# Kernel optimization log

Hardware: AMD Instinct MI355X
Metric: run time of the kernel (lower is better)

Reference implementation:

```python
import jax, jax.numpy as jnp
import numpy as np

ALPHA = 0.2  # LeakyReLU negative slope
NEG_INF = -9e15


def setup_inputs() -> dict:
    key = jax.random.key(0)
    k1, k2, k3, k4 = jax.random.split(key, 4)
    B, N, F_in, F_out = 8, 2048, 256, 128
    h = jax.random.normal(k1, (B, N, F_in), dtype=jnp.float32)
    adj = jax.random.randint(k2, (B, N, N), 0, 2, dtype=jnp.int32)
    # xavier_uniform with gain=1.414
    def xavier(k, shape, gain=1.414):
        fan_in, fan_out = shape[0], shape[1]
        limit = gain * np.sqrt(6.0 / (fan_in + fan_out))
        return jax.random.uniform(k, shape, jnp.float32, -limit, limit)
    W = xavier(k3, (F_in, F_out))
    a = xavier(k4, (2 * F_out, 1))
    return {"h": h, "adj": adj, "W": W, "a": a}


def reference(h, adj, W, a):
    # h: [B,N,F_in], adj: [B,N,N], W: [F_in,F_out], a: [2*F_out,1]
    Wh = jnp.einsum('bnf,fe->bne', h, W)  # [B,N,E]
    E = Wh.shape[-1]
    a_src, a_dst = a[:E, 0], a[E:, 0]
    # e[b,i,j] = leakyrelu(Wh[b,i].a_src + Wh[b,j].a_dst)  (additive decomposition
    # of a @ concat(Wh_i, Wh_j) -- same math, no [B,N,N,2E] intermediate)
    s_src = Wh @ a_src  # [B,N]
    s_dst = Wh @ a_dst  # [B,N]
    e = jax.nn.leaky_relu(s_src[:, :, None] + s_dst[:, None, :], negative_slope=ALPHA)
    e = jnp.where(adj > 0, e, NEG_INF)
    attention = jax.nn.softmax(e, axis=2)  # [B,N,N]
    # dropout p=0.0 / eval mode -> identity
    h_prime = jnp.einsum('bij,bje->bie', attention, Wh)
    return jax.nn.elu(h_prime)  # concat=True
```

## Files before the change

### kernel.cpp

```cpp
#include <hip/hip_runtime.h>
#include <hip/hip_bf16.h>

#define GAT_ALPHA 0.2f
#define LOG2E 1.4426950408889634f

typedef float f32x4 __attribute__((ext_vector_type(4)));
typedef int   i32x4 __attribute__((ext_vector_type(4)));
typedef short bf16x8 __attribute__((ext_vector_type(8)));

static constexpr int Nn  = 2048;
static constexpr int FIN = 256;
static constexpr int FO  = 128;

static __device__ __forceinline__ unsigned short f2bf(float x) {
    __hip_bfloat16 h = __float2bfloat16(x);
    return __builtin_bit_cast(unsigned short, h);
}
static __device__ __forceinline__ float bf2f(unsigned short u) {
    unsigned int v = ((unsigned int)u) << 16;
    return __builtin_bit_cast(float, v);
}

__global__ __launch_bounds__(256) void gat_prep(
        const float* __restrict__ W, const float* __restrict__ a,
        float* __restrict__ wa, unsigned int* __restrict__ md_key)
{
    __shared__ float pr[32][8];
    __shared__ float pd[32][8];
    const int t = threadIdx.x;
    const int kl = t >> 3, seg = t & 7;
    const int k = blockIdx.x * 32 + kl;
    float ps = 0.f, pv = 0.f;
    const float* wr = W + (size_t)k * FO + seg * 16;
    #pragma unroll
    for (int f = 0; f < 16; f += 4) {
        f32x4 wv = *(const f32x4*)(wr + f);
        f32x4 as = *(const f32x4*)(a + seg * 16 + f);
        f32x4 ad = *(const f32x4*)(a + FO + seg * 16 + f);
        ps += wv[0]*as[0] + wv[1]*as[1] + wv[2]*as[2] + wv[3]*as[3];
        pv += wv[0]*ad[0] + wv[1]*ad[1] + wv[2]*ad[2] + wv[3]*ad[3];
    }
    pr[kl][seg] = ps; pd[kl][seg] = pv;
    __syncthreads();
    if (t < 32) {
        float s = 0.f, d = 0.f;
        #pragma unroll
        for (int j = 0; j < 8; ++j) { s += pr[t][j]; d += pd[t][j]; }
        wa[blockIdx.x * 32 + t]       = s;
        wa[256 + blockIdx.x * 32 + t] = d;
    }
    if (blockIdx.x == 0 && t < 8) md_key[t] = 0u;
}

__global__ __launch_bounds__(256) void gat_wh(
        const float* __restrict__ h, const float* __restrict__ W,
        const float* __restrict__ wa, unsigned short* __restrict__ WhT,
        float* __restrict__ s_src, float* __restrict__ s_dst,
        unsigned int* __restrict__ md_key)
{
    __shared__ unsigned short WT[FO][264];
    __shared__ float wal[512];
    __shared__ float sred[64][4][2];
    __shared__ float red64[64];
    const int t  = threadIdx.x;
    const int b  = blockIdx.x & 7;
    const int n0 = (blockIdx.x >> 3) << 6;

    if (t < 128) *(f32x4*)&wal[t * 4] = *(const f32x4*)&wa[t * 4];
    #pragma unroll
    for (int c = 0; c < 32; ++c) {
        int flat = c * 1024 + t * 4;
        int k = flat >> 7, f = flat & 127;
        f32x4 wv = *(const f32x4*)&W[flat];
        WT[f + 0][k] = f2bf(wv[0]);
        WT[f + 1][k] = f2bf(wv[1]);
        WT[f + 2][k] = f2bf(wv[2]);
        WT[f + 3][k] = f2bf(wv[3]);
    }
    __syncthreads();

    {
        const int row = t >> 2, seg = t & 3;
        const float* hp  = h + ((size_t)(b * Nn + n0 + row)) * FIN + seg * 64;
        const float* was = &wal[seg * 64];
        const float* wad = &wal[256 + seg * 64];
        float ps = 0.f, pv = 0.f;
        #pragma unroll
        for (int j = 0; j < 64; j += 4) {
            f32x4 hv = *(const f32x4*)(hp + j);
            f32x4 sv = *(const f32x4*)(was + j);
            f32x4 dv = *(const f32x4*)(wad + j);
            ps += hv[0]*sv[0] + hv[1]*sv[1] + hv[2]*sv[2] + hv[3]*sv[3];
            pv += hv[0]*dv[0] + hv[1]*dv[1] + hv[2]*dv[2] + hv[3]*dv[3];
        }
        sred[row][seg][0] = ps;
        sred[row][seg][1] = pv;
    }
    __syncthreads();
    if (t < 64) {
        float s = sred[t][0][0] + sred[t][1][0] + sred[t][2][0] + sred[t][3][0];
        float d = sred[t][0][1] + sred[t][1][1] + sred[t][2][1] + sred[t][3][1];
        s_src[b * Nn + n0 + t] = s;
        s_dst[b * Nn + n0 + t] = d;
        red64[t] = d;
    }
    __syncthreads();
    if (t < 16) red64[t] = fmaxf(fmaxf(red64[t], red64[t + 16]),
                                 fmaxf(red64[t + 32], red64[t + 48]));
    __syncthreads();
    if (t == 0) {
        float m = red64[0];
        #pragma unroll
        for (int j = 1; j < 16; ++j) m = fmaxf(m, red64[j]);
        unsigned int bits = __builtin_bit_cast(unsigned int, m);
        unsigned int key  = (bits & 0x80000000u) ? ~bits : (bits | 0x80000000u);
        atomicMax(md_key + b, key);
    }

    const int w = t >> 6, lane = t & 63, n16 = lane & 15, quad = lane >> 4;
    const float* ha = h + ((size_t)(b * Nn + n0 + w * 16 + n16)) * FIN + quad * 8;
    f32x4 acc[8] = {};
    #pragma unroll
    for (int ks = 0; ks < 8; ++ks) {
        f32x4 h0 = *(const f32x4*)(ha + ks * 32);
        f32x4 h1 = *(const f32x4*)(ha + ks * 32 + 4);
        bf16x8 af;
        af[0] = (short)f2bf(h0[0]); af[1] = (short)f2bf(h0[1]);
        af[2] = (short)f2bf(h0[2]); af[3] = (short)f2bf(h0[3]);
        af[4] = (short)f2bf(h1[0]); af[5] = (short)f2bf(h1[1]);
        af[6] = (short)f2bf(h1[2]); af[7] = (short)f2bf(h1[3]);
        #pragma unroll
        for (int nt = 0; nt < 8; ++nt) {
            bf16x8 bfr = *(const bf16x8*)&WT[nt * 16 + n16][ks * 32 + quad * 8];
            acc[nt] = __builtin_amdgcn_mfma_f32_16x16x32_bf16(af, bfr, acc[nt], 0, 0, 0);
        }
    }
    #pragma unroll
    for (int nt = 0; nt < 8; ++nt) {
        ushort4 pk;
        pk.x = f2bf(acc[nt][0]); pk.y = f2bf(acc[nt][1]);
        pk.z = f2bf(acc[nt][2]); pk.w = f2bf(acc[nt][3]);
        *(ushort4*)&WhT[((size_t)(b * FO + nt * 16 + n16)) * Nn + n0 + w * 16 + quad * 4] = pk;
    }
}

__global__ __launch_bounds__(256, 3) void gat_attn(
        const int* __restrict__ adj, const unsigned short* __restrict__ WhT,
        const float* __restrict__ s_src, const float* __restrict__ s_dst,
        const unsigned int* __restrict__ md_key, float* __restrict__ out)
{
    constexpr int WS = 136;
    constexpr int PS = 136;
    constexpr int AS = 132;
    __shared__ __align__(16) unsigned short whs[128 * WS];
    __shared__ __align__(16) unsigned short psT[32 * PS];
    __shared__ float l_red[32];
    float* accbuf = (float*)whs;

    const int t = threadIdx.x, w = t >> 6, lane = t & 63;
    const int n16 = lane & 15, quad = lane >> 4;
    const int b  = blockIdx.x & 7;
    const int i0 = (blockIdx.x >> 3) << 5;
    const int r  = t >> 3;
    const int jg = t & 7;

    if (t < 32) l_red[t] = 0.f;

    const unsigned int key = md_key[b];
    const unsigned int mb  = (key & 0x80000000u) ? (key ^ 0x80000000u) : ~key;
    const float mdb = __builtin_bit_cast(float, mb);
    const float ssr = s_src[b * Nn + i0 + r];
    const float tm  = ssr + mdb;
    const float mi  = fmaxf(tm, GAT_ALPHA * tm) * LOG2E;
    const float ssL = ssr * LOG2E;

    const int* arow = adj + ((size_t)(b * Nn + i0 + r)) * Nn;
    const float* dB = s_dst + b * Nn;
    const unsigned short* wrow = WhT + ((size_t)(b * FO + (w << 5))) * Nn;
    const int fsub = lane >> 4;
    const int jc16 = lane & 15;

    f32x4 acc[2][8] = {};
    float ls = 0.f;

    i32x4 pa[4];
    #pragma unroll
    for (int k = 0; k < 4; ++k) pa[k] = *(const i32x4*)(arow + (jg << 2) + (k << 5));

    for (int s = 0; s < 16; ++s) {
        const int j0 = s << 7;
        bf16x8 wreg[8];
        #pragma unroll
        for (int i = 0; i < 8; ++i)
            wreg[i] = *(const bf16x8*)(wrow + (size_t)((i << 2) + fsub) * Nn + j0 + (jc16 << 3));
        float e16[16];
        #pragma unroll
        for (int k = 0; k < 4; ++k) {
            f32x4 dv = *(const f32x4*)(dB + j0 + (jg << 2) + (k << 5));
            #pragma unroll
            for (int j = 0; j < 4; ++j) {
                float u  = __builtin_fmaf(dv[j], LOG2E, ssL);
                float lr = fmaxf(u, GAT_ALPHA * u);
                float e  = __builtin_amdgcn_exp2f(lr - mi);
                e16[k * 4 + j] = (pa[k][j] > 0) ? e : 0.f;
            }
        }
        const int jn = (s < 15) ? (j0 + 128) : 0;
        #pragma unroll
        for (int k = 0; k < 4; ++k) pa[k] = *(const i32x4*)(arow + jn + (jg << 2) + (k << 5));
        #pragma unroll
        for (int k = 0; k < 4; ++k) {
            unsigned short u0 = f2bf(e16[k*4+0]), u1 = f2bf(e16[k*4+1]);
            unsigned short u2 = f2bf(e16[k*4+2]), u3 = f2bf(e16[k*4+3]);
            ls += bf2f(u0) + bf2f(u1) + bf2f(u2) + bf2f(u3);
            ushort4 pk; pk.x = u0; pk.y = u1; pk.z = u2; pk.w = u3;
            *(ushort4*)&psT[r * PS + (jg << 2) + (k << 5)] = pk;
        }
        #pragma unroll
        for (int i = 0; i < 8; ++i)
            *(bf16x8*)&whs[((w << 5) + (i << 2) + fsub) * WS + (jc16 << 3)] = wreg[i];
        __syncthreads();
        bf16x8 bfr[8];
        #pragma unroll
        for (int nt = 0; nt < 8; ++nt)
            bfr[nt] = *(const bf16x8*)&whs[((nt << 4) + n16) * WS + (w << 5) + (quad << 3)];
        #pragma unroll
        for (int ig = 0; ig < 2; ++ig) {
            bf16x8 af = *(const bf16x8*)&psT[((ig << 4) + n16) * PS + (w << 5) + (quad << 3)];
            #pragma unroll
            for (int nt = 0; nt < 8; ++nt)
                acc[ig][nt] = __builtin_amdgcn_mfma_f32_16x16x32_bf16(af, bfr[nt], acc[ig][nt], 0, 0, 0);
        }
        __syncthreads();
    }

    atomicAdd(&l_red[r], ls);
    if (w < 2) {
        #pragma unroll
        for (int ig = 0; ig < 2; ++ig)
            #pragma unroll
            for (int nt = 0; nt < 8; ++nt)
                #pragma unroll
                for (int rr = 0; rr < 4; ++rr)
                    accbuf[(size_t)w * 32 * AS + (ig * 16 + quad * 4 + rr) * AS + nt * 16 + n16] = acc[ig][nt][rr];
    }
    __syncthreads();
    if (w >= 2) {
        #pragma unroll
        for (int ig = 0; ig < 2; ++ig)
            #pragma unroll
            for (int nt = 0; nt < 8; ++nt)
                #pragma unroll
                for (int rr = 0; rr < 4; ++rr)
                    accbuf[(size_t)(w - 2) * 32 * AS + (ig * 16 + quad * 4 + rr) * AS + nt * 16 + n16] += acc[ig][nt][rr];
    }
    __syncthreads();
    float* ob = out + ((size_t)(b * Nn + i0)) * FO;
    #pragma unroll
    for (int c = 0; c < 4; ++c) {
        int flat = c * 1024 + t * 4;
        int m = flat >> 7, f = flat & 127;
        f32x4 v0 = *(const f32x4*)&accbuf[(size_t)m * AS + f];
        f32x4 v1 = *(const f32x4*)&accbuf[(size_t)32 * AS + m * AS + f];
        float l = l_red[m];
        f32x4 o;
        #pragma unroll
        for (int j = 0; j < 4; ++j) {
            float x = (v0[j] + v1[j]) / l;
            o[j] = x > 0.f ? x : expm1f(x);
        }
        *(f32x4*)&ob[(size_t)m * FO + f] = o;
    }
}

extern "C" void kernel_launch(void* const* d_in, const int* in_sizes, int n_in,
                              void* d_out, int out_size, void* d_ws, size_t ws_size,
                              hipStream_t stream)
{
    const float* h   = (const float*)d_in[0];
    const int*   adj = (const int*)d_in[1];
    const float* W   = (const float*)d_in[2];
    const float* a   = (const float*)d_in[3];
    float* out = (float*)d_out;

    char* ws = (char*)d_ws;
    unsigned short* WhT = (unsigned short*)ws;
    float* s_src        = (float*)(ws + 4194304);
    float* s_dst        = (float*)(ws + 4259840);
    float* wa           = (float*)(ws + 4325376);
    unsigned int* md_key= (unsigned int*)(ws + 4327424);

    hipLaunchKernelGGL(gat_prep, dim3(8),   dim3(256), 0, stream, W, a, wa, md_key);
    hipLaunchKernelGGL(gat_wh,   dim3(256), dim3(256), 0, stream, h, W, wa, WhT, s_src, s_dst, md_key);
    hipLaunchKernelGGL(gat_attn, dim3(512), dim3(256), 0, stream, adj, WhT, s_src, s_dst, md_key, out);
}
```

Before: 234.5 us.

## Pack adjacency into bitmask and pre-block Wh for barrier-free attention loop

Adds a pre-pass kernel that compresses the int32 adjacency matrix into one bit per edge. gat_wh now writes Wh in an MFMA-fragment-blocked layout, so gat_attn loads B fragments straight from global memory instead of staging them through LDS. The attention kernel builds the softmax numerators directly in registers in A-fragment layout, using s_dst and the mask bits held in LDS, which removes the per-step __syncthreads and the LDS round trips. The full adjacency is still read once by the extra pass (128MB), and occupancy bounds change from 3 to 2 blocks per CU.

```diff
diff --git a/kernel.cpp b/kernel.cpp
--- a/kernel.cpp
+++ b/kernel.cpp
@@ -19,6 +19,29 @@
 static __device__ __forceinline__ float bf2f(unsigned short u) {
     unsigned int v = ((unsigned int)u) << 16;
     return __builtin_bit_cast(float, v);
+}
+
+__global__ __launch_bounds__(256) void gat_adjbits(
+        const int* __restrict__ adj, unsigned char* __restrict__ mbytes)
+{
+    const int g = blockIdx.x * 256 + threadIdx.x;
+    #pragma unroll 4
+    for (int it = 0; it < 16; ++it) {
+        const size_t bi = (size_t)it * 262144 + (size_t)g;
+        const int* p = adj + (bi << 3);
+        i32x4 v0 = *(const i32x4*)(p);
+        i32x4 v1 = *(const i32x4*)(p + 4);
+        unsigned int m = 0;
+        m |= (v0[0] > 0) ? 1u   : 0u;
+        m |= (v0[1] > 0) ? 2u   : 0u;
+        m |= (v0[2] > 0) ? 4u   : 0u;
+        m |= (v0[3] > 0) ? 8u   : 0u;
+        m |= (v1[0] > 0) ? 16u  : 0u;
+        m |= (v1[1] > 0) ? 32u  : 0u;
+        m |= (v1[2] > 0) ? 64u  : 0u;
+        m |= (v1[3] > 0) ? 128u : 0u;
+        mbytes[bi] = (unsigned char)m;
+    }
 }
 
 __global__ __launch_bounds__(256) void gat_prep(
@@ -54,7 +77,7 @@
 
 __global__ __launch_bounds__(256) void gat_wh(
         const float* __restrict__ h, const float* __restrict__ W,
-        const float* __restrict__ wa, unsigned short* __restrict__ WhT,
+        const float* __restrict__ wa, unsigned short* __restrict__ WhB,
         float* __restrict__ s_src, float* __restrict__ s_dst,
         unsigned int* __restrict__ md_key)
 {
@@ -135,106 +158,108 @@
             acc[nt] = __builtin_amdgcn_mfma_f32_16x16x32_bf16(af, bfr, acc[nt], 0, 0, 0);
         }
     }
-    #pragma unroll
-    for (int nt = 0; nt < 8; ++nt) {
-        ushort4 pk;
-        pk.x = f2bf(acc[nt][0]); pk.y = f2bf(acc[nt][1]);
-        pk.z = f2bf(acc[nt][2]); pk.w = f2bf(acc[nt][3]);
-        *(ushort4*)&WhT[((size_t)(b * FO + nt * 16 + n16)) * Nn + n0 + w * 16 + quad * 4] = pk;
-    }
-}
-
-__global__ __launch_bounds__(256, 3) void gat_attn(
-        const int* __restrict__ adj, const unsigned short* __restrict__ WhT,
+    {
+        const int K   = (n0 >> 5) + (w >> 1);
+        const int jl  = ((w & 1) << 4) + (quad << 2);
+        const int q2  = jl >> 3;
+        const int off = jl & 7;
+        unsigned short* wpb = WhB + (((size_t)(b * 64 + K)) << 12)
+                                  + (((q2 << 4) + n16) << 3) + off;
+        #pragma unroll
+        for (int nt = 0; nt < 8; ++nt) {
+            ushort4 pk;
+            pk.x = f2bf(acc[nt][0]); pk.y = f2bf(acc[nt][1]);
+            pk.z = f2bf(acc[nt][2]); pk.w = f2bf(acc[nt][3]);
+            *(ushort4*)(wpb + ((size_t)nt << 9)) = pk;
+        }
+    }
+}
+
+__global__ __launch_bounds__(256, 2) void gat_attn(
+        const unsigned long long* __restrict__ mbits,
+        const unsigned short* __restrict__ WhB,
         const float* __restrict__ s_src, const float* __restrict__ s_dst,
         const unsigned int* __restrict__ md_key, float* __restrict__ out)
 {
-    constexpr int WS = 136;
-    constexpr int PS = 136;
-    constexpr int AS = 132;
-    __shared__ __align__(16) unsigned short whs[128 * WS];
-    __shared__ __align__(16) unsigned short psT[32 * PS];
+    __shared__ float sdl[2048];
+    __shared__ unsigned long long msk[32][34];
+    __shared__ float accbuf[2][32][132];
     __shared__ float l_red[32];
-    float* accbuf = (float*)whs;
 
     const int t = threadIdx.x, w = t >> 6, lane = t & 63;
     const int n16 = lane & 15, quad = lane >> 4;
     const int b  = blockIdx.x & 7;
     const int i0 = (blockIdx.x >> 3) << 5;
-    const int r  = t >> 3;
-    const int jg = t & 7;
-
+
+    #pragma unroll
+    for (int c = 0; c < 2; ++c) {
+        int idx = (c << 10) + (t << 2);
+        *(f32x4*)&sdl[idx] = *(const f32x4*)&s_dst[b * Nn + idx];
+    }
+    {
+        int row = t >> 3, cc = t & 7;
+        const unsigned long long* mr = mbits + ((size_t)(b * Nn + i0 + row) << 5) + (cc << 2);
+        ulonglong2 m0 = *(const ulonglong2*)(mr);
+        ulonglong2 m1 = *(const ulonglong2*)(mr + 2);
+        msk[row][(cc << 2) + 0] = m0.x; msk[row][(cc << 2) + 1] = m0.y;
+        msk[row][(cc << 2) + 2] = m1.x; msk[row][(cc << 2) + 3] = m1.y;
+    }
     if (t < 32) l_red[t] = 0.f;
+    __syncthreads();
 
     const unsigned int key = md_key[b];
-    const unsigned int mb  = (key & 0x80000000u) ? (key ^ 0x80000000u) : ~key;
-    const float mdb = __builtin_bit_cast(float, mb);
-    const float ssr = s_src[b * Nn + i0 + r];
-    const float tm  = ssr + mdb;
-    const float mi  = fmaxf(tm, GAT_ALPHA * tm) * LOG2E;
-    const float ssL = ssr * LOG2E;
-
-    const int* arow = adj + ((size_t)(b * Nn + i0 + r)) * Nn;
-    const float* dB = s_dst + b * Nn;
-    const unsigned short* wrow = WhT + ((size_t)(b * FO + (w << 5))) * Nn;
-    const int fsub = lane >> 4;
-    const int jc16 = lane & 15;
-
+    const unsigned int mb_ = (key & 0x80000000u) ? (key ^ 0x80000000u) : ~key;
+    const float mdb = __builtin_bit_cast(float, mb_);
+    float ssL[2], mi[2];
+    #pragma unroll
+    for (int ig = 0; ig < 2; ++ig) {
+        float ss = s_src[b * Nn + i0 + (ig << 4) + n16];
+        float tm = ss + mdb;
+        mi[ig]  = fmaxf(tm, GAT_ALPHA * tm) * LOG2E;
+        ssL[ig] = ss * LOG2E;
+    }
+
+    const unsigned short* wb = WhB + ((size_t)b << 18) + ((size_t)lane << 3);
     f32x4 acc[2][8] = {};
-    float ls = 0.f;
-
-    i32x4 pa[4];
-    #pragma unroll
-    for (int k = 0; k < 4; ++k) pa[k] = *(const i32x4*)(arow + (jg << 2) + (k << 5));
+    float ls0 = 0.f, ls1 = 0.f;
 
     for (int s = 0; s < 16; ++s) {
-        const int j0 = s << 7;
-        bf16x8 wreg[8];
-        #pragma unroll
-        for (int i = 0; i < 8; ++i)
-            wreg[i] = *(const bf16x8*)(wrow + (size_t)((i << 2) + fsub) * Nn + j0 + (jc16 << 3));
-        float e16[16];
-        #pragma unroll
-        for (int k = 0; k < 4; ++k) {
-            f32x4 dv = *(const f32x4*)(dB + j0 + (jg << 2) + (k << 5));
+        const int ks = (s << 2) | w;
+        const int kw = ks << 5;
+        const unsigned short* wp = wb + ((size_t)ks << 12);
+        bf16x8 bfr[8];
+        #pragma unroll
+        for (int nt = 0; nt < 8; ++nt)
+            bfr[nt] = *(const bf16x8*)(wp + (nt << 9));
+        f32x4 d0 = *(const f32x4*)&sdl[kw + (quad << 3)];
+        f32x4 d1 = *(const f32x4*)&sdl[kw + (quad << 3) + 4];
+        float dv[8] = {d0[0],d0[1],d0[2],d0[3],d1[0],d1[1],d1[2],d1[3]};
+        #pragma unroll
+        for (int ig = 0; ig < 2; ++ig) {
+            unsigned long long m64 = msk[(ig << 4) + n16][kw >> 6];
+            unsigned int mh = (kw & 32) ? (unsigned int)(m64 >> 32) : (unsigned int)m64;
+            mh >>= (quad << 3);
+            bf16x8 af;
+            float lsl = 0.f;
             #pragma unroll
-            for (int j = 0; j < 4; ++j) {
-                float u  = __builtin_fmaf(dv[j], LOG2E, ssL);
+            for (int jj = 0; jj < 8; ++jj) {
+                float u  = __builtin_fmaf(dv[jj], LOG2E, ssL[ig]);
                 float lr = fmaxf(u, GAT_ALPHA * u);
-                float e  = __builtin_amdgcn_exp2f(lr - mi);
-                e16[k * 4 + j] = (pa[k][j] > 0) ? e : 0.f;
+                float e  = __builtin_amdgcn_exp2f(lr - mi[ig]);
+                e = ((mh >> jj) & 1u) ? e : 0.f;
+                unsigned short ub = f2bf(e);
+                af[jj] = (short)ub;
+                lsl += bf2f(ub);
             }
-        }
-        const int jn = (s < 15) ? (j0 + 128) : 0;
-        #pragma unroll
-        for (int k = 0; k < 4; ++k) pa[k] = *(const i32x4*)(arow + jn + (jg << 2) + (k << 5));
-        #pragma unroll
-        for (int k = 0; k < 4; ++k) {
-            unsigned short u0 = f2bf(e16[k*4+0]), u1 = f2bf(e16[k*4+1]);
-            unsigned short u2 = f2bf(e16[k*4+2]), u3 = f2bf(e16[k*4+3]);
-            ls += bf2f(u0) + bf2f(u1) + bf2f(u2) + bf2f(u3);
-            ushort4 pk; pk.x = u0; pk.y = u1; pk.z = u2; pk.w = u3;
-            *(ushort4*)&psT[r * PS + (jg << 2) + (k << 5)] = pk;
-        }
-        #pragma unroll
-        for (int i = 0; i < 8; ++i)
-            *(bf16x8*)&whs[((w << 5) + (i << 2) + fsub) * WS + (jc16 << 3)] = wreg[i];
-        __syncthreads();
-        bf16x8 bfr[8];
-        #pragma unroll
-        for (int nt = 0; nt < 8; ++nt)
-            bfr[nt] = *(const bf16x8*)&whs[((nt << 4) + n16) * WS + (w << 5) + (quad << 3)];
-        #pragma unroll
-        for (int ig = 0; ig < 2; ++ig) {
-            bf16x8 af = *(const bf16x8*)&psT[((ig << 4) + n16) * PS + (w << 5) + (quad << 3)];
+            if (ig == 0) ls0 += lsl; else ls1 += lsl;
             #pragma unroll
             for (int nt = 0; nt < 8; ++nt)
                 acc[ig][nt] = __builtin_amdgcn_mfma_f32_16x16x32_bf16(af, bfr[nt], acc[ig][nt], 0, 0, 0);
         }
-        __syncthreads();
-    }
-
-    atomicAdd(&l_red[r], ls);
+    }
+
+    atomicAdd(&l_red[n16], ls0);
+    atomicAdd(&l_red[16 + n16], ls1);
     if (w < 2) {
         #pragma unroll
         for (int ig = 0; ig < 2; ++ig)
@@ -242,7 +267,7 @@
             for (int nt = 0; nt < 8; ++nt)
                 #pragma unroll
                 for (int rr = 0; rr < 4; ++rr)
-                    accbuf[(size_t)w * 32 * AS + (ig * 16 + quad * 4 + rr) * AS + nt * 16 + n16] = acc[ig][nt][rr];
+                    accbuf[w][(ig << 4) + (quad << 2) + rr][(nt << 4) + n16] = acc[ig][nt][rr];
     }
     __syncthreads();
     if (w >= 2) {
@@ -252,16 +277,16 @@
             for (int nt = 0; nt < 8; ++nt)
                 #pragma unroll
                 for (int rr = 0; rr < 4; ++rr)
-                    accbuf[(size_t)(w - 2) * 32 * AS + (ig * 16 + quad * 4 + rr) * AS + nt * 16 + n16] += acc[ig][nt][rr];
+                    accbuf[w - 2][(ig << 4) + (quad << 2) + rr][(nt << 4) + n16] += acc[ig][nt][rr];
     }
     __syncthreads();
     float* ob = out + ((size_t)(b * Nn + i0)) * FO;
     #pragma unroll
     for (int c = 0; c < 4; ++c) {
-        int flat = c * 1024 + t * 4;
+        int flat = (c << 10) + (t << 2);
         int m = flat >> 7, f = flat & 127;
-        f32x4 v0 = *(const f32x4*)&accbuf[(size_t)m * AS + f];
-        f32x4 v1 = *(const f32x4*)&accbuf[(size_t)32 * AS + m * AS + f];
+        f32x4 v0 = *(const f32x4*)&accbuf[0][m][f];
+        f32x4 v1 = *(const f32x4*)&accbuf[1][m][f];
         float l = l_red[m];
         f32x4 o;
         #pragma unroll
@@ -284,13 +309,16 @@
     float* out = (float*)d_out;
 
     char* ws = (char*)d_ws;
-    unsigned short* WhT = (unsigned short*)ws;
-    float* s_src        = (float*)(ws + 4194304);
-    float* s_dst        = (float*)(ws + 4259840);
-    float* wa           = (float*)(ws + 4325376);
-    unsigned int* md_key= (unsigned int*)(ws + 4327424);
-
-    hipLaunchKernelGGL(gat_prep, dim3(8),   dim3(256), 0, stream, W, a, wa, md_key);
-    hipLaunchKernelGGL(gat_wh,   dim3(256), dim3(256), 0, stream, h, W, wa, WhT, s_src, s_dst, md_key);
-    hipLaunchKernelGGL(gat_attn, dim3(512), dim3(256), 0, stream, adj, WhT, s_src, s_dst, md_key, out);
-}
+    unsigned short* WhB   = (unsigned short*)ws;
+    unsigned char*  mbyte = (unsigned char*)(ws + 4194304);
+    float* s_src          = (float*)(ws + 8388608);
+    float* s_dst          = (float*)(ws + 8454144);
+    float* wa             = (float*)(ws + 8519680);
+    unsigned int* md_key  = (unsigned int*)(ws + 8521728);
+
+    hipLaunchKernelGGL(gat_adjbits, dim3(1024), dim3(256), 0, stream, adj, mbyte);
+    hipLaunchKernelGGL(gat_prep,    dim3(8),    dim3(256), 0, stream, W, a, wa, md_key);
+    hipLaunchKernelGGL(gat_wh,      dim3(256),  dim3(256), 0, stream, h, W, wa, WhB, s_src, s_dst, md_key);
+    hipLaunchKernelGGL(gat_attn,    dim3(512),  dim3(256), 0, stream,
+                       (const unsigned long long*)mbyte, WhB, s_src, s_dst, md_key, out);
+}
```

New measurement: 250.5 us. 1.07x slower.
